# Performance work log

Hardware: AMD Instinct MI355X
Metric: run time of the kernel (lower is better)

## Reference

```python
import jax, jax.numpy as jnp
import numpy as np

B = 4096        # graphs
N0 = 32         # nodes per graph
N = B * N0      # 131072 nodes
EP = 128        # edges per graph
E = B * EP      # 524288 edges
H, C = 2, 64    # heads, per-head channels
D = H * C       # 128
K1, K2, K3 = 29, 27, 25  # ceil(0.9*32), ceil(0.9*29), ceil(0.9*27)


def setup_inputs() -> dict:
    key = jax.random.key(0)
    ks = jax.random.split(key, 8)
    x = jax.random.normal(ks[0], (N, 41), jnp.float32)
    g = jnp.repeat(jnp.arange(B, dtype=jnp.int32), EP)
    src = g * N0 + jax.random.randint(ks[1], (E,), 0, N0, jnp.int32)
    dst = g * N0 + jax.random.randint(ks[2], (E,), 0, N0, jnp.int32)
    edge_index = jnp.stack([src, dst])
    edge_attr = jax.random.normal(ks[3], (E, 10), jnp.float32)
    batch = jnp.repeat(jnp.arange(B, dtype=jnp.int32), N0)

    def lin(k, i, o):
        return jax.random.normal(k, (i, o), jnp.float32) / np.float32(np.sqrt(i))

    p = {"x": x, "edge_index": edge_index, "edge_attr": edge_attr, "batch": batch}
    fins = {1: 41, 2: D, 3: D}
    for li in (1, 2, 3):
        sub = jax.random.split(ks[3 + li], 6)
        p[f"W{li}"] = lin(sub[0], fins[li], D)
        p[f"We{li}"] = lin(sub[1], 10, D)
        p[f"as{li}"] = jax.random.normal(sub[2], (H, C), jnp.float32) * 0.1
        p[f"ad{li}"] = jax.random.normal(sub[3], (H, C), jnp.float32) * 0.1
        p[f"ae{li}"] = jax.random.normal(sub[4], (H, C), jnp.float32) * 0.1
        p[f"b{li}"] = jnp.zeros((D,), jnp.float32)
        p[f"g{li}"] = jnp.ones((D,), jnp.float32)
        p[f"be{li}"] = jnp.zeros((D,), jnp.float32)
        p[f"pw{li}"] = jax.random.normal(sub[5], (D,), jnp.float32)
    sub = jax.random.split(ks[7], 2)
    p["fw1"] = lin(sub[0], D, 64)
    p["fb1"] = jnp.zeros((64,), jnp.float32)
    p["fw2"] = lin(sub[1], 64, 1)
    p["fb2"] = jnp.zeros((1,), jnp.float32)
    return p


def gat_conv(x, src, dst, edge_attr, node_mask, edge_mask, W, We, a_s, a_d, a_e, b):
    # PyG GATConv w/ edge_dim, add_self_loops=True, fill_value='mean'
    emf = edge_mask.astype(x.dtype)
    loop_attr = jax.ops.segment_sum(edge_attr * emf[:, None], dst, num_segments=N)
    loop_attr = loop_attr / jnp.maximum(jax.ops.segment_sum(emf, dst, num_segments=N), 1.0)[:, None]
    idx = jnp.arange(N, dtype=src.dtype)
    s = jnp.concatenate([src, idx])
    d = jnp.concatenate([dst, idx])
    ea = jnp.concatenate([edge_attr, loop_attr], axis=0)
    msk = jnp.concatenate([edge_mask, node_mask])
    h = (x @ W).reshape(N, H, C)                       # [N,H,C]
    eh = (ea @ We).reshape(-1, H, C)                   # [E+N,H,C]
    alpha = (h * a_s).sum(-1)[s] + (h * a_d).sum(-1)[d] + (eh * a_e).sum(-1)
    alpha = jax.nn.leaky_relu(alpha, 0.2)              # [E+N,H]
    alpha = jnp.where(msk[:, None], alpha, -1e9)
    mx = jax.ops.segment_max(alpha, d, num_segments=N)  # segment softmax over dst
    p = jnp.where(msk[:, None], jnp.exp(alpha - mx[d]), 0.0)
    den = jax.ops.segment_sum(p, d, num_segments=N)
    w = p / jnp.maximum(den[d], 1e-16)
    out = jax.ops.segment_sum(w[:, :, None] * h[s], d, num_segments=N)
    return out.reshape(N, D) + b


def masked_bn(x, nm, gamma, beta, eps=1e-5):
    m = nm.astype(x.dtype)[:, None]
    n = jnp.maximum(m.sum(), 1.0)
    mu = (x * m).sum(0) / n
    var = (jnp.square(x - mu) * m).sum(0) / n
    return gamma * (x - mu) * jax.lax.rsqrt(var + eps) + beta


def topk_pool(x, w, nm, k):
    sc = (x @ w) / jnp.linalg.norm(w)                  # [N]
    sg = jnp.where(nm, sc, -1e9).reshape(B, N0)
    _, idx = jax.lax.top_k(sg, k)                      # per-graph top-k
    nm2 = jnp.zeros((B, N0), bool).at[jnp.arange(B)[:, None], idx].set(True).reshape(-1)
    xn = jnp.where(nm2[:, None], x * jnp.tanh(sc)[:, None], 0.0)
    return xn, nm2


def graph_mean(x, nm, batch):
    m = nm.astype(x.dtype)
    s = jax.ops.segment_sum(x * m[:, None], batch, num_segments=B)
    c = jax.ops.segment_sum(m, batch, num_segments=B)
    return s / jnp.maximum(c, 1.0)[:, None]


def _forward(x, edge_index, edge_attr, batch,
             W1, We1, as1, ad1, ae1, b1, g1, be1, pw1,
             W2, We2, as2, ad2, ae2, b2, g2, be2, pw2,
             W3, We3, as3, ad3, ae3, b3, g3, be3, pw3,
             fw1, fb1, fw2, fb2):
    src, dst = edge_index[0], edge_index[1]
    nm = jnp.ones((N,), bool)
    em = jnp.ones((E,), bool)
    layers = [(W1, We1, as1, ad1, ae1, b1, g1, be1, pw1, K1),
              (W2, We2, as2, ad2, ae2, b2, g2, be2, pw2, K2),
              (W3, We3, as3, ad3, ae3, b3, g3, be3, pw3, K3)]
    reads = []
    for (W, We, a_s, a_d, a_e, b, g, be, pw, k) in layers:
        x = gat_conv(x, src, dst, edge_attr, nm, em, W, We, a_s, a_d, a_e, b)
        x = jax.nn.relu(masked_bn(x, nm, g, be))
        x, nm = topk_pool(x, pw, nm, k)
        em = em & nm[src] & nm[dst]
        reads.append(graph_mean(x, nm, batch))
    z = reads[0] + reads[1] + reads[2]
    z = jax.nn.relu(z @ fw1 + fb1)
    return z @ fw2 + fb2


def reference(x, edge_index, edge_attr, batch,
              W1, We1, as1, ad1, ae1, b1, g1, be1, pw1,
              W2, We2, as2, ad2, ae2, b2, g2, be2, pw2,
              W3, We3, as3, ad3, ae3, b3, g3, be3, pw3,
              fw1, fb1, fw2, fb2):
    return _forward(x, edge_index, edge_attr, batch,
                    W1, We1, as1, ad1, ae1, b1, g1, be1, pw1,
                    W2, We2, as2, ad2, ae2, b2, g2, be2, pw2,
                    W3, We3, as3, ad3, ae3, b3, g3, be3, pw3,
                    fw1, fb1, fw2, fb2)
```

## Files before the change

kernel.cpp:

```cpp
#include <hip/hip_runtime.h>

#define NN 131072
#define NG 4096
#define NE 524288

__device__ __forceinline__ float lrelu(float a){ return a>=0.f ? a : 0.2f*a; }

template<int K, int PMODE, int KSEL>
__global__ __launch_bounds__(256) void pool_gemm_kernel(
    const float* __restrict__ Xin, float* bufA, unsigned char* nmg,
    const float* __restrict__ stat,
    const float* __restrict__ gamma, const float* __restrict__ beta,
    const float* __restrict__ Wg,
    float* zacc)
{
    constexpr int XSZ = (K == 41) ? 64 * 44 : 64 * 128;
    __shared__ float xs[XSZ];
    __shared__ float scS[64], tsS[64];
    __shared__ int   nmlS[64];

    int tid = threadIdx.x;
    long row0 = (long)blockIdx.x * 64;
    int g0 = blockIdx.x * 2;

    if (PMODE == 0) {
        for (int i = tid; i < 64 * 41; i += 256) {
            int r = i / 41, c = i - r * 41;
            xs[r * 44 + c] = Xin[row0 * 41 + i];
        }
    } else {
        for (int i = tid; i < 2048; i += 256) {
            int r = i >> 5, c4 = i & 31, dc = c4 * 4;
            float4 v = *(const float4*)&bufA[(row0 + r) * 128 + dc];
            v.x = fmaxf(gamma[dc    ] * (v.x - stat[dc    ]) * stat[128 + dc    ] + beta[dc    ], 0.f);
            v.y = fmaxf(gamma[dc + 1] * (v.y - stat[dc + 1]) * stat[128 + dc + 1] + beta[dc + 1], 0.f);
            v.z = fmaxf(gamma[dc + 2] * (v.z - stat[dc + 2]) * stat[128 + dc + 2] + beta[dc + 2], 0.f);
            v.w = fmaxf(gamma[dc + 3] * (v.w - stat[dc + 3]) * stat[128 + dc + 3] + beta[dc + 3], 0.f);
            *(float4*)&xs[r * 128 + ((c4 ^ (r & 7)) << 2)] = v;
        }
        if (tid < 64) nmlS[tid] = (PMODE == 1) ? 1 : (int)nmg[g0 * 32 + tid];
    }
    __syncthreads();

    if (PMODE > 0) {
        {
            int node = tid >> 2, l4 = tid & 3, kk = node & 7;
            float s = 0.f;
            for (int m = 0; m < 32; m++)
                s += xs[node * 128 + ((m ^ kk) << 2) + l4] * stat[256 + 4 * m + l4];
            s += __shfl_xor(s, 2); s += __shfl_xor(s, 1);
            if (l4 == 0) scS[node] = s;
        }
        __syncthreads();
        if (tid < 64) {
            int gp = tid >> 5, n = tid & 31;
            float sn = nmlS[tid] ? scS[tid] : -1e9f;
            int cnt = 0;
            for (int j = 0; j < 32; j++) {
                float sj = nmlS[gp * 32 + j] ? scS[gp * 32 + j] : -1e9f;
                cnt += (sj > sn || (sj == sn && j < n)) ? 1 : 0;
            }
            int sl = (cnt < KSEL) ? 1 : 0;
            nmg[g0 * 32 + tid] = (unsigned char)sl;
            tsS[tid] = sl ? tanhf(scS[tid]) : 0.f;
        }
        __syncthreads();
        {
            int gp = tid >> 7, d = tid & 127, c4 = d >> 2, j = d & 3;
            float s = 0.f;
            for (int n = 0; n < 32; n++) {
                int r = gp * 32 + n;
                s += tsS[r] * xs[r * 128 + ((c4 ^ (r & 7)) << 2) + j];
            }
            zacc[(long)(g0 + gp) * 128 + d] += s * (1.0f / (float)KSEL);
        }
    }

    int lane = tid & 63;
    int wv = __builtin_amdgcn_readfirstlane(tid >> 6);
    const float* __restrict__ Wb = Wg + wv * 32;

    float accv[32];
#pragma unroll
    for (int c = 0; c < 32; c++) accv[c] = 0.f;

    constexpr int KM4 = (K / 4) * 4;
#pragma unroll 2
    for (int k0 = 0; k0 < KM4; k0 += 4) {
        float4 xv;
        if (PMODE == 0) {
            xv = *(const float4*)&xs[lane * 44 + k0];
        } else {
            xv = *(const float4*)&xs[lane * 128 + ((((k0 >> 2) ^ (lane & 7))) << 2)];
        }
        {
            const float* Wr = Wb + (k0 + 0) * 128;
#pragma unroll
            for (int c = 0; c < 32; c++) accv[c] += xv.x * Wr[c];
        }
        {
            const float* Wr = Wb + (k0 + 1) * 128;
#pragma unroll
            for (int c = 0; c < 32; c++) accv[c] += xv.y * Wr[c];
        }
        {
            const float* Wr = Wb + (k0 + 2) * 128;
#pragma unroll
            for (int c = 0; c < 32; c++) accv[c] += xv.z * Wr[c];
        }
        {
            const float* Wr = Wb + (k0 + 3) * 128;
#pragma unroll
            for (int c = 0; c < 32; c++) accv[c] += xv.w * Wr[c];
        }
    }
    for (int k = KM4; k < K; k++) {
        float xk = (PMODE == 0)
            ? xs[lane * 44 + k]
            : xs[lane * 128 + (((k >> 2) ^ (lane & 7)) << 2) + (k & 3)];
        const float* Wr = Wb + k * 128;
#pragma unroll
        for (int c = 0; c < 32; c++) accv[c] += xk * Wr[c];
    }

    {
        float t = 1.f;
        if (PMODE > 0) t = tsS[lane];
        float* orow = &bufA[(row0 + lane) * 128 + wv * 32];
#pragma unroll
        for (int cc = 0; cc < 8; cc++)
            *(float4*)&orow[cc * 4] = make_float4(
                accv[cc * 4 + 0] * t, accv[cc * 4 + 1] * t,
                accv[cc * 4 + 2] * t, accv[cc * 4 + 3] * t);
    }
}

__global__ __launch_bounds__(256) void attn_kernel(
    float* bufA,
    const int* __restrict__ srcp, const int* __restrict__ dstp,
    const float* __restrict__ EA,
    const unsigned char* __restrict__ nmg,
    const float* __restrict__ stat,
    const float* __restrict__ as_, const float* __restrict__ ad_,
    const float* __restrict__ bb,
    float* sums)
{
    __shared__ float hs[32 * 128];
    __shared__ float Wm[2 * 32 * 36];
    __shared__ float scr[320];
    __shared__ unsigned char nmlS[32];

    int g = blockIdx.x, tid = threadIdx.x;
    long gb = (long)g * 4096;

    float ea0 = 0.f, ea1 = 0.f;
    int myls = 0, myld = 0;
    if (tid < 128) {
        myls = srcp[g * 128 + tid] & 31;
        myld = dstp[g * 128 + tid] & 31;
        const float* ep = EA + (long)(g * 128 + tid) * 10;
#pragma unroll
        for (int j = 0; j < 10; j++) { float v = ep[j]; ea0 += v * stat[384 + j]; ea1 += v * stat[394 + j]; }
    }
    for (int i = tid; i < 2304; i += 256) Wm[i] = 0.f;
    if (tid < 96) scr[128 + tid] = 0.f;
    if (tid < 32) nmlS[tid] = nmg[g * 32 + tid];
#pragma unroll
    for (int k = 0; k < 4; k++) {
        int i = tid + 256 * k, r = i >> 5, c4 = i & 31;
        *(float4*)&hs[r * 128 + ((c4 ^ (r & 7)) << 2)] =
            *(const float4*)&bufA[gb + (long)i * 4];
    }
    __syncthreads();

    {
        int node = tid >> 3, l8 = tid & 7, rb = node * 128, k = node & 7;
        float s0 = 0, s1 = 0, d0 = 0, d1 = 0;
#pragma unroll
        for (int m = 0; m < 8; m++) {
            int c = l8 + 8 * m, c4 = c >> 2, j = c & 3;
            int o0 = rb + ((c4 ^ k) << 2) + j;
            float h0 = hs[o0], h1 = hs[o0 + 64];
            s0 += h0 * as_[c];      s1 += h1 * as_[64 + c];
            d0 += h0 * ad_[c];      d1 += h1 * ad_[64 + c];
        }
        s0 += __shfl_xor(s0, 4); s0 += __shfl_xor(s0, 2); s0 += __shfl_xor(s0, 1);
        s1 += __shfl_xor(s1, 4); s1 += __shfl_xor(s1, 2); s1 += __shfl_xor(s1, 1);
        d0 += __shfl_xor(d0, 4); d0 += __shfl_xor(d0, 2); d0 += __shfl_xor(d0, 1);
        d1 += __shfl_xor(d1, 4); d1 += __shfl_xor(d1, 2); d1 += __shfl_xor(d1, 1);
        if (l8 == 0) {
            scr[node * 2] = s0;      scr[node * 2 + 1] = s1;
            scr[64 + node * 2] = d0; scr[64 + node * 2 + 1] = d1;
        }
    }
    int mymk = 0;
    if (tid < 128) {
        mymk = (int)nmlS[myls] & (int)nmlS[myld];
        if (mymk) {
            atomicAdd(&scr[128 + myld * 2], ea0);
            atomicAdd(&scr[128 + myld * 2 + 1], ea1);
            atomicAdd(&scr[192 + myld], 1.f);
        }
    }
    __syncthreads();

    if (tid < 128) {
        if (mymk) {
            float p0 = __expf(lrelu(scr[myls * 2]     + scr[64 + myld * 2]     + ea0));
            float p1 = __expf(lrelu(scr[myls * 2 + 1] + scr[64 + myld * 2 + 1] + ea1));
            atomicAdd(&Wm[myls * 36 + myld], p0);
            atomicAdd(&Wm[1152 + myls * 36 + myld], p1);
        }
    } else if (tid < 192) {
        int t2 = tid - 128, n = t2 >> 1, h = t2 & 1;
        if (nmlS[n]) {
            float c = scr[192 + n]; c = (c > 0.f) ? c : 1.f;
            float ps = __expf(lrelu(scr[n * 2 + h] + scr[64 + n * 2 + h] + scr[128 + n * 2 + h] / c));
            atomicAdd(&Wm[h * 1152 + n * 36 + n], ps);
        }
    }
    __syncthreads();

    if (tid < 64) {
        int n = tid & 31, h = tid >> 5;
        const float* Wh = &Wm[h * 1152 + n];
        float den = 0.f;
#pragma unroll 8
        for (int s = 0; s < 32; s++) den += Wh[s * 36];
        scr[256 + h * 32 + n] = 1.f / fmaxf(den, 1e-16f);
    } else if (tid < 128) {
        *(float4*)&scr[(tid - 64) * 4] = make_float4(0.f, 0.f, 0.f, 0.f);
    }
    __syncthreads();

    {
        int d = tid & 127, h = d >> 6, nb = tid >> 7;
        int c4 = d >> 2, j = d & 3;
        const float* Wh = &Wm[h * 1152 + nb * 16];
        float acc[16];
#pragma unroll
        for (int i = 0; i < 16; i++) acc[i] = 0.f;
        for (int s = 0; s < 32; s++) {
            float hv = hs[s * 128 + ((c4 ^ (s & 7)) << 2) + j];
            float4 w0 = *(const float4*)&Wh[s * 36];
            float4 w1 = *(const float4*)&Wh[s * 36 + 4];
            float4 w2 = *(const float4*)&Wh[s * 36 + 8];
            float4 w3 = *(const float4*)&Wh[s * 36 + 12];
            acc[0]  += w0.x * hv; acc[1]  += w0.y * hv; acc[2]  += w0.z * hv; acc[3]  += w0.w * hv;
            acc[4]  += w1.x * hv; acc[5]  += w1.y * hv; acc[6]  += w1.z * hv; acc[7]  += w1.w * hv;
            acc[8]  += w2.x * hv; acc[9]  += w2.y * hv; acc[10] += w2.z * hv; acc[11] += w2.w * hv;
            acc[12] += w3.x * hv; acc[13] += w3.y * hv; acc[14] += w3.z * hv; acc[15] += w3.w * hv;
        }
        float bv = bb[d];
        float sp = 0.f, sq = 0.f;
#pragma unroll
        for (int i = 0; i < 16; i++) {
            int n = nb * 16 + i;
            float v = acc[i] * scr[256 + h * 32 + n] + bv;
            bufA[gb + n * 128 + d] = v;
            if (nmlS[n]) { sp += v; sq += v * v; }
        }
        atomicAdd(&scr[d], sp);
        atomicAdd(&scr[128 + d], sq);
    }
    __syncthreads();

    if (tid < 128) {
        int rep = (g & 31) * 256;
        atomicAdd(&sums[rep + tid], scr[tid]);
        atomicAdd(&sums[rep + 128 + tid], scr[128 + tid]);
    }
}

__global__ __launch_bounds__(128) void setup_kernel(
    float* sums, float* stat, const float* __restrict__ We, const float* __restrict__ ae)
{
    int t = threadIdx.x;
    for (int i = t; i < 32 * 256; i += 128) sums[i] = 0.f;
    if (t < 20) {
        int h = t / 10, j = t - 10 * h;
        float s = 0.f;
        for (int c = 0; c < 64; c++) s += We[j * 128 + h * 64 + c] * ae[h * 64 + c];
        stat[384 + t] = s;
    }
}

__global__ __launch_bounds__(128) void finalize_kernel(
    float* sums, float n, const float* __restrict__ pw, float* stat,
    const float* __restrict__ Wen, const float* __restrict__ aen)
{
    int d = threadIdx.x;
    float s1 = 0.f, s2 = 0.f;
#pragma unroll
    for (int r = 0; r < 32; r++) { s1 += sums[r * 256 + d]; s2 += sums[r * 256 + 128 + d]; }
    float mean = s1 / n;
    float var = s2 / n - mean * mean;
    if (var < 0.f) var = 0.f;
    float rstd = rsqrtf(var + 1e-5f);
    float p = pw[d];
    float q = p * p;
#pragma unroll
    for (int o = 32; o >= 1; o >>= 1) q += __shfl_xor(q, o);
    __shared__ float w2[2];
    if ((d & 63) == 0) w2[d >> 6] = q;
    __syncthreads();
    float nrm = sqrtf(w2[0] + w2[1]);
    stat[d] = mean; stat[128 + d] = rstd; stat[256 + d] = p / nrm;
    if (d < 20) {
        int h = d / 10, j = d - 10 * h;
        float s = 0.f;
        for (int c = 0; c < 64; c++) s += Wen[j * 128 + h * 64 + c] * aen[h * 64 + c];
        stat[384 + d] = s;
    }
    for (int i = d; i < 32 * 256; i += 128) sums[i] = 0.f;
}

__global__ __launch_bounds__(256) void final_kernel(
    const float* __restrict__ bufA, const unsigned char* __restrict__ nmg,
    const float* __restrict__ stat,
    const float* __restrict__ gamma, const float* __restrict__ beta,
    const float* __restrict__ zacc,
    const float* __restrict__ fw1, const float* __restrict__ fb1,
    const float* __restrict__ fw2, const float* __restrict__ fb2,
    float* __restrict__ out)
{
    __shared__ float xs[32 * 132], zt[128], hred[64], scS[32], tsS[32];
    __shared__ int nmlS[32];
    int g = blockIdx.x, tid = threadIdx.x;
    long gb = (long)g * 4096;

    if (tid < 32) nmlS[tid] = (int)nmg[g * 32 + tid];
    for (int i = tid; i < 1024; i += 256) {
        int r = i >> 5, dc = (i & 31) * 4;
        float4 v = *(const float4*)&bufA[gb + i * 4];
        v.x = fmaxf(gamma[dc    ] * (v.x - stat[dc    ]) * stat[128 + dc    ] + beta[dc    ], 0.f);
        v.y = fmaxf(gamma[dc + 1] * (v.y - stat[dc + 1]) * stat[128 + dc + 1] + beta[dc + 1], 0.f);
        v.z = fmaxf(gamma[dc + 2] * (v.z - stat[dc + 2]) * stat[128 + dc + 2] + beta[dc + 2], 0.f);
        v.w = fmaxf(gamma[dc + 3] * (v.w - stat[dc + 3]) * stat[128 + dc + 3] + beta[dc + 3], 0.f);
        *(float4*)&xs[r * 132 + dc] = v;
    }
    __syncthreads();

    {
        int node = tid >> 3, l8 = tid & 7;
        float s = 0.f;
        for (int m = 0; m < 16; m++) { int c = l8 + 8 * m; s += xs[node * 132 + c] * stat[256 + c]; }
        s += __shfl_xor(s, 4); s += __shfl_xor(s, 2); s += __shfl_xor(s, 1);
        if (l8 == 0) scS[node] = s;
    }
    __syncthreads();

    if (tid < 32) {
        float sn = nmlS[tid] ? scS[tid] : -1e9f;
        int cnt = 0;
        for (int j = 0; j < 32; j++) {
            float sj = nmlS[j] ? scS[j] : -1e9f;
            cnt += (sj > sn || (sj == sn && j < tid)) ? 1 : 0;
        }
        tsS[tid] = (cnt < 25) ? tanhf(scS[tid]) : 0.f;
    }
    __syncthreads();

    if (tid < 128) {
        float s = 0.f;
        for (int n = 0; n < 32; n++) s += xs[n * 132 + tid] * tsS[n];
        zt[tid] = zacc[(long)g * 128 + tid] + s * (1.0f / 25.0f);
    }
    __syncthreads();

    {
        int j = tid >> 2, p = tid & 3;
        float s = 0.f;
        for (int d = p * 32; d < p * 32 + 32; d++) s += zt[d] * fw1[d * 64 + j];
        s += __shfl_xor(s, 1); s += __shfl_xor(s, 2);
        if (p == 0) hred[j] = fmaxf(s + fb1[j], 0.f) * fw2[j];
    }
    __syncthreads();
    if (tid < 64) {
        float v = hred[tid];
#pragma unroll
        for (int o = 32; o >= 1; o >>= 1) v += __shfl_xor(v, o);
        if (tid == 0) out[g] = v + fb2[0];
    }
}

extern "C" void kernel_launch(void* const* d_in, const int* in_sizes, int n_in,
                              void* d_out, int out_size, void* d_ws, size_t ws_size,
                              hipStream_t stream)
{
    const float* X0 = (const float*)d_in[0];
    const int*   EI = (const int*)d_in[1];
    const float* EA = (const float*)d_in[2];
    const int* srcp = EI;
    const int* dstp = EI + NE;

    const float* W1  = (const float*)d_in[4];  const float* We1 = (const float*)d_in[5];
    const float* as1 = (const float*)d_in[6];  const float* ad1 = (const float*)d_in[7];
    const float* ae1 = (const float*)d_in[8];  const float* b1  = (const float*)d_in[9];
    const float* g1  = (const float*)d_in[10]; const float* be1 = (const float*)d_in[11];
    const float* pw1 = (const float*)d_in[12];
    const float* W2  = (const float*)d_in[13]; const float* We2 = (const float*)d_in[14];
    const float* as2 = (const float*)d_in[15]; const float* ad2 = (const float*)d_in[16];
    const float* ae2 = (const float*)d_in[17]; const float* b2  = (const float*)d_in[18];
    const float* g2  = (const float*)d_in[19]; const float* be2 = (const float*)d_in[20];
    const float* pw2 = (const float*)d_in[21];
    const float* W3  = (const float*)d_in[22]; const float* We3 = (const float*)d_in[23];
    const float* as3 = (const float*)d_in[24]; const float* ad3 = (const float*)d_in[25];
    const float* ae3 = (const float*)d_in[26]; const float* b3  = (const float*)d_in[27];
    const float* g3  = (const float*)d_in[28]; const float* be3 = (const float*)d_in[29];
    const float* pw3 = (const float*)d_in[30];
    const float* fw1 = (const float*)d_in[31]; const float* fb1 = (const float*)d_in[32];
    const float* fw2 = (const float*)d_in[33]; const float* fb2 = (const float*)d_in[34];

    float* bufA = (float*)d_ws;
    float* z    = bufA + (size_t)NN * 128;
    float* sums = z + (size_t)NG * 128;
    float* stat = sums + 32 * 256;
    unsigned char* nmg = (unsigned char*)(stat + 512);

    hipMemsetAsync(nmg, 1, NN, stream);
    hipMemsetAsync(z, 0, (size_t)NG * 128 * sizeof(float), stream);
    setup_kernel<<<1, 128, 0, stream>>>(sums, stat, We1, ae1);

    pool_gemm_kernel<41, 0, 1><<<NN / 64, 256, 0, stream>>>(
        X0, bufA, nmg, stat, g1, be1, W1, z);
    attn_kernel<<<NG, 256, 0, stream>>>(bufA, srcp, dstp, EA, nmg, stat, as1, ad1, b1, sums);
    finalize_kernel<<<1, 128, 0, stream>>>(sums, 131072.f, pw1, stat, We2, ae2);

    pool_gemm_kernel<128, 1, 29><<<NN / 64, 256, 0, stream>>>(
        X0, bufA, nmg, stat, g1, be1, W2, z);
    attn_kernel<<<NG, 256, 0, stream>>>(bufA, srcp, dstp, EA, nmg, stat, as2, ad2, b2, sums);
    finalize_kernel<<<1, 128, 0, stream>>>(sums, 4096.f * 29.f, pw2, stat, We3, ae3);

    pool_gemm_kernel<128, 2, 27><<<NN / 64, 256, 0, stream>>>(
        X0, bufA, nmg, stat, g2, be2, W3, z);
    attn_kernel<<<NG, 256, 0, stream>>>(bufA, srcp, dstp, EA, nmg, stat, as3, ad3, b3, sums);
    finalize_kernel<<<1, 128, 0, stream>>>(sums, 4096.f * 27.f, pw3, stat, We3, ae3);

    final_kernel<<<NG, 256, 0, stream>>>(
        bufA, nmg, stat, g3, be3, z, fw1, fb1, fw2, fb2, (float*)d_out);
}
```

Before: 558.2 us.

## Use 512-thread blocks in pool_gemm with 16 columns per wave and padded smem

The pool/GEMM kernel now launches 512 threads per 64-row tile, so each of 8 waves computes 16 output columns instead of 32. Per-thread accumulators shrink from 32 to 16 registers, which should raise occupancy and latency hiding. The XOR-swizzled shared-memory layout is replaced by a row pitch of 132, padded to avoid bank conflicts, and the score reduction is reworked to use 8 lanes per node. The trade-off is that more threads each reload the same x row from shared memory, and each wave does less work per block.

```diff
diff --git a/kernel.cpp b/kernel.cpp
--- a/kernel.cpp
+++ b/kernel.cpp
@@ -7,15 +7,15 @@
 __device__ __forceinline__ float lrelu(float a){ return a>=0.f ? a : 0.2f*a; }
 
 template<int K, int PMODE, int KSEL>
-__global__ __launch_bounds__(256) void pool_gemm_kernel(
+__global__ __launch_bounds__(512) void pool_gemm_kernel(
     const float* __restrict__ Xin, float* bufA, unsigned char* nmg,
     const float* __restrict__ stat,
     const float* __restrict__ gamma, const float* __restrict__ beta,
     const float* __restrict__ Wg,
     float* zacc)
 {
-    constexpr int XSZ = (K == 41) ? 64 * 44 : 64 * 128;
-    __shared__ float xs[XSZ];
+    constexpr int XP = (K == 41) ? 44 : 132;
+    __shared__ float xs[64 * XP];
     __shared__ float scS[64], tsS[64];
     __shared__ int   nmlS[64];
 
@@ -24,19 +24,19 @@
     int g0 = blockIdx.x * 2;
 
     if (PMODE == 0) {
-        for (int i = tid; i < 64 * 41; i += 256) {
+        for (int i = tid; i < 64 * 41; i += 512) {
             int r = i / 41, c = i - r * 41;
             xs[r * 44 + c] = Xin[row0 * 41 + i];
         }
     } else {
-        for (int i = tid; i < 2048; i += 256) {
-            int r = i >> 5, c4 = i & 31, dc = c4 * 4;
+        for (int i = tid; i < 2048; i += 512) {
+            int r = i >> 5, dc = (i & 31) * 4;
             float4 v = *(const float4*)&bufA[(row0 + r) * 128 + dc];
             v.x = fmaxf(gamma[dc    ] * (v.x - stat[dc    ]) * stat[128 + dc    ] + beta[dc    ], 0.f);
             v.y = fmaxf(gamma[dc + 1] * (v.y - stat[dc + 1]) * stat[128 + dc + 1] + beta[dc + 1], 0.f);
             v.z = fmaxf(gamma[dc + 2] * (v.z - stat[dc + 2]) * stat[128 + dc + 2] + beta[dc + 2], 0.f);
             v.w = fmaxf(gamma[dc + 3] * (v.w - stat[dc + 3]) * stat[128 + dc + 3] + beta[dc + 3], 0.f);
-            *(float4*)&xs[r * 128 + ((c4 ^ (r & 7)) << 2)] = v;
+            *(float4*)&xs[r * XP + dc] = v;
         }
         if (tid < 64) nmlS[tid] = (PMODE == 1) ? 1 : (int)nmg[g0 * 32 + tid];
     }
@@ -44,12 +44,12 @@
 
     if (PMODE > 0) {
         {
-            int node = tid >> 2, l4 = tid & 3, kk = node & 7;
+            int node = tid >> 3, l8 = tid & 7;
             float s = 0.f;
-            for (int m = 0; m < 32; m++)
-                s += xs[node * 128 + ((m ^ kk) << 2) + l4] * stat[256 + 4 * m + l4];
-            s += __shfl_xor(s, 2); s += __shfl_xor(s, 1);
-            if (l4 == 0) scS[node] = s;
+#pragma unroll
+            for (int m = 0; m < 16; m++) { int c = l8 + 8 * m; s += xs[node * XP + c] * stat[256 + c]; }
+            s += __shfl_xor(s, 4); s += __shfl_xor(s, 2); s += __shfl_xor(s, 1);
+            if (l8 == 0) scS[node] = s;
         }
         __syncthreads();
         if (tid < 64) {
@@ -65,70 +65,60 @@
             tsS[tid] = sl ? tanhf(scS[tid]) : 0.f;
         }
         __syncthreads();
-        {
-            int gp = tid >> 7, d = tid & 127, c4 = d >> 2, j = d & 3;
+        if (tid < 256) {
+            int gp = tid >> 7, d = tid & 127;
             float s = 0.f;
-            for (int n = 0; n < 32; n++) {
-                int r = gp * 32 + n;
-                s += tsS[r] * xs[r * 128 + ((c4 ^ (r & 7)) << 2) + j];
-            }
+            for (int n = 0; n < 32; n++) s += tsS[gp * 32 + n] * xs[(gp * 32 + n) * XP + d];
             zacc[(long)(g0 + gp) * 128 + d] += s * (1.0f / (float)KSEL);
         }
     }
 
     int lane = tid & 63;
     int wv = __builtin_amdgcn_readfirstlane(tid >> 6);
-    const float* __restrict__ Wb = Wg + wv * 32;
-
-    float accv[32];
-#pragma unroll
-    for (int c = 0; c < 32; c++) accv[c] = 0.f;
+    const float* __restrict__ Wb = Wg + wv * 16;
+
+    float accv[16];
+#pragma unroll
+    for (int c = 0; c < 16; c++) accv[c] = 0.f;
 
     constexpr int KM4 = (K / 4) * 4;
 #pragma unroll 2
     for (int k0 = 0; k0 < KM4; k0 += 4) {
-        float4 xv;
-        if (PMODE == 0) {
-            xv = *(const float4*)&xs[lane * 44 + k0];
-        } else {
-            xv = *(const float4*)&xs[lane * 128 + ((((k0 >> 2) ^ (lane & 7))) << 2)];
-        }
+        float4 xv = *(const float4*)&xs[lane * XP + k0];
         {
             const float* Wr = Wb + (k0 + 0) * 128;
 #pragma unroll
-            for (int c = 0; c < 32; c++) accv[c] += xv.x * Wr[c];
+            for (int c = 0; c < 16; c++) accv[c] += xv.x * Wr[c];
         }
         {
             const float* Wr = Wb + (k0 + 1) * 128;
 #pragma unroll
-            for (int c = 0; c < 32; c++) accv[c] += xv.y * Wr[c];
+            for (int c = 0; c < 16; c++) accv[c] += xv.y * Wr[c];
         }
         {
             const float* Wr = Wb + (k0 + 2) * 128;
 #pragma unroll
-            for (int c = 0; c < 32; c++) accv[c] += xv.z * Wr[c];
+            for (int c = 0; c < 16; c++) accv[c] += xv.z * Wr[c];
         }
         {
             const float* Wr = Wb + (k0 + 3) * 128;
 #pragma unroll
-            for (int c = 0; c < 32; c++) accv[c] += xv.w * Wr[c];
+            for (int c = 0; c < 16; c++) accv[c] += xv.w * Wr[c];
         }
     }
     for (int k = KM4; k < K; k++) {
-        float xk = (PMODE == 0)
-            ? xs[lane * 44 + k]
-            : xs[lane * 128 + (((k >> 2) ^ (lane & 7)) << 2) + (k & 3)];
+        float xk = xs[lane * XP + k];
         const float* Wr = Wb + k * 128;
 #pragma unroll
-        for (int c = 0; c < 32; c++) accv[c] += xk * Wr[c];
+        for (int c = 0; c < 16; c++) accv[c] += xk * Wr[c];
     }
 
     {
         float t = 1.f;
         if (PMODE > 0) t = tsS[lane];
-        float* orow = &bufA[(row0 + lane) * 128 + wv * 32];
-#pragma unroll
-        for (int cc = 0; cc < 8; cc++)
+        float* orow = &bufA[(row0 + lane) * 128 + wv * 16];
+#pragma unroll
+        for (int cc = 0; cc < 4; cc++)
             *(float4*)&orow[cc * 4] = make_float4(
                 accv[cc * 4 + 0] * t, accv[cc * 4 + 1] * t,
                 accv[cc * 4 + 2] * t, accv[cc * 4 + 3] * t);
@@ -422,17 +412,17 @@
     hipMemsetAsync(z, 0, (size_t)NG * 128 * sizeof(float), stream);
     setup_kernel<<<1, 128, 0, stream>>>(sums, stat, We1, ae1);
 
-    pool_gemm_kernel<41, 0, 1><<<NN / 64, 256, 0, stream>>>(
+    pool_gemm_kernel<41, 0, 1><<<NN / 64, 512, 0, stream>>>(
         X0, bufA, nmg, stat, g1, be1, W1, z);
     attn_kernel<<<NG, 256, 0, stream>>>(bufA, srcp, dstp, EA, nmg, stat, as1, ad1, b1, sums);
     finalize_kernel<<<1, 128, 0, stream>>>(sums, 131072.f, pw1, stat, We2, ae2);
 
-    pool_gemm_kernel<128, 1, 29><<<NN / 64, 256, 0, stream>>>(
+    pool_gemm_kernel<128, 1, 29><<<NN / 64, 512, 0, stream>>>(
         X0, bufA, nmg, stat, g1, be1, W2, z);
     attn_kernel<<<NG, 256, 0, stream>>>(bufA, srcp, dstp, EA, nmg, stat, as2, ad2, b2, sums);
     finalize_kernel<<<1, 128, 0, stream>>>(sums, 4096.f * 29.f, pw2, stat, We3, ae3);
 
-    pool_gemm_kernel<128, 2, 27><<<NN / 64, 256, 0, stream>>>(
+    pool_gemm_kernel<128, 2, 27><<<NN / 64, 512, 0, stream>>>(
         X0, bufA, nmg, stat, g2, be2, W3, z);
     attn_kernel<<<NG, 256, 0, stream>>>(bufA, srcp, dstp, EA, nmg, stat, as3, ad3, b3, sums);
     finalize_kernel<<<1, 128, 0, stream>>>(sums, 4096.f * 27.f, pw3, stat, We3, ae3);
```

Measured after the change: 512.4 us, median of 3. 1.09x faster.
